# Kernel tuning notes

Measured on AMD Instinct MI355X. Metric: run time of the kernel, lower is better.

The kernel has to match this reference:

```python
import jax, jax.numpy as jnp
import numpy as np

LOG2PI = float(np.log(2.0 * np.pi))
T, S, D, K = 1024, 512, 32, 64


def setup_inputs() -> dict:
    key = jax.random.key(0)
    k0, k1, k2, k3, k4 = jax.random.split(key, 5)
    data = jax.random.normal(k0, (T, S, D), dtype=jnp.float32)  # packed time-major
    ip = jax.random.uniform(k1, (K,), dtype=jnp.float32)
    initial_probs = ip / ip.sum()
    A = jax.random.uniform(k2, (K, K), dtype=jnp.float32)
    transition_probs = A / A.sum(-1, keepdims=True)  # row-stochastic
    means = jax.random.normal(k3, (K, D), dtype=jnp.float32)
    covars = jax.random.uniform(k4, (K, D), dtype=jnp.float32) * 0.5 + 0.5  # positive diag
    return {"data": data, "initial_probs": initial_probs,
            "transition_probs": transition_probs, "means": means, "covars": covars}


def _emission_probs(data, means, covars):
    # Gaussian diag-covariance densities, [T, S, K], without materializing [T,S,K,D].
    inv = 1.0 / covars  # [K, D]
    quad = (jnp.einsum('tsd,kd->tsk', data * data, inv)
            - 2.0 * jnp.einsum('tsd,kd->tsk', data, means * inv)
            + (means * means * inv).sum(-1))  # [T, S, K]
    logp = -0.5 * (quad + jnp.log(covars).sum(-1) + data.shape[-1] * LOG2PI)
    return jnp.exp(logp)


def reference(data, initial_probs, transition_probs, means, covars):
    probs = _emission_probs(data, means, covars)  # [T, S, K]
    # t = 0: alpha = normalize(initial * emission)
    a0 = initial_probs * probs[0]
    d0 = a0.sum(-1, keepdims=True)
    alpha0 = a0 / d0
    log_denom0 = jnp.log(d0)  # [S, 1]

    def step(carry, p_t):
        alpha, log_denom = carry
        a = p_t * (alpha @ transition_probs)  # [S, K]
        d = a.sum(-1, keepdims=True)
        return (a / d, log_denom + jnp.log(d)), None

    (alpha, log_denom), _ = jax.lax.scan(step, (alpha0, log_denom0), probs[1:])
    log_likeli = jax.nn.logsumexp(jnp.log(alpha) + log_denom, axis=-1).sum()
    return alpha, -log_likeli
```

## Files before the change

kernel.cpp:

```cpp
#include <hip/hip_runtime.h>
#include <hip/hip_fp16.h>
#include <math.h>

#define TT 1024
#define SS 512
#define DD 32
#define KK 64

#define LOG2PI_F 1.8378770664093453f

#define QSEQ 16
#define NSEG 16
#define SEGLEN (TT / NSEG)
#define BURN 64

#define PBUF_BYTES ((size_t)TT * SS * KK * 2)
#define EM_WPB 4
#define EM_BLOCKS 2048
#define NWAVES (EM_BLOCKS * EM_WPB)

typedef float v2f __attribute__((ext_vector_type(2)));
typedef float f32x4 __attribute__((ext_vector_type(4)));
typedef _Float16 h8 __attribute__((ext_vector_type(8)));

__device__ __forceinline__ v2f fma2(v2f a, v2f b, v2f c) {
#if __has_builtin(__builtin_elementwise_fma)
    return __builtin_elementwise_fma(a, b, c);
#else
    v2f r; r.x = fmaf(a.x, b.x, c.x); r.y = fmaf(a.y, b.y, c.y); return r;
#endif
}

template <int CTRL, int RMASK>
__device__ __forceinline__ float dpp_max(float x) {
    int xi = __float_as_int(x);
    int t = __builtin_amdgcn_update_dpp(xi, xi, CTRL, RMASK, 0xf, false);
    return fmaxf(x, __int_as_float(t));
}
__device__ __forceinline__ float wave_reduce_max(float x) {
    x = dpp_max<0x111, 0xf>(x);
    x = dpp_max<0x112, 0xf>(x);
    x = dpp_max<0x114, 0xf>(x);
    x = dpp_max<0x118, 0xf>(x);
    x = dpp_max<0x142, 0xa>(x);
    x = dpp_max<0x143, 0xc>(x);
    return __int_as_float(__builtin_amdgcn_readlane(__float_as_int(x), 63));
}
template <int N>
__device__ __forceinline__ float dpp_ror_add(float x) {
    int xi = __float_as_int(x);
    int t = __builtin_amdgcn_update_dpp(xi, xi, 0x120 + N, 0xf, 0xf, false);
    return x + __int_as_float(t);
}
__device__ __forceinline__ float rowsum16(float x) {
    x = dpp_ror_add<8>(x);
    x = dpp_ror_add<4>(x);
    x = dpp_ror_add<2>(x);
    x = dpp_ror_add<1>(x);
    return x;
}

__global__ __launch_bounds__(EM_WPB * 64)
__attribute__((amdgpu_waves_per_eu(1, 3)))
void emission_kernel(
    const float* __restrict__ data,
    const float* __restrict__ means,
    const float* __restrict__ covars,
    __half* __restrict__ pbuf,
    float* __restrict__ mpart)
{
    const int k  = threadIdx.x & 63;
    const int w  = threadIdx.x >> 6;
    const int wv = blockIdx.x * EM_WPB + w;

    v2f w2[DD / 2], m2[DD / 2];
    float c0 = DD * LOG2PI_F;
#pragma unroll
    for (int d = 0; d < DD; ++d) {
        float c = covars[k * DD + d];
        ((float*)w2)[d] = 1.0f / c;
        ((float*)m2)[d] = means[k * DD + d];
        c0 += __logf(c);
    }

    __shared__ __align__(16) float4 xst[EM_WPB][2][64];

    const int base = wv * 64;
    const float4* dsrc = (const float4*)(data + (size_t)base * DD);

    float4 xr = dsrc[k];
    xst[w][0][k] = xr;
    __builtin_amdgcn_wave_barrier();

    float macc = 0.0f;
    int cur = 0;

    for (int b = 0; b < 8; ++b) {
        const int bn = (b + 1 < 8) ? (b + 1) : 7;
        xr = dsrc[bn * 64 + k];

        const float* xb = (const float*)&xst[w][cur][0];
#pragma unroll
        for (int i = 0; i < 8; i += 2) {
            const float4* x0q = (const float4*)(xb + i * DD);
            const float4* x1q = (const float4*)(xb + (i + 1) * DD);
            v2f p00 = {0,0}, p01 = {0,0}, p10 = {0,0}, p11 = {0,0};
#pragma unroll
            for (int d4 = 0; d4 < DD / 4; ++d4) {
                float4 x0 = x0q[d4];
                float4 x1 = x1q[d4];
                v2f xa0; xa0.x = x0.x; xa0.y = x0.y;
                v2f xb0; xb0.x = x0.z; xb0.y = x0.w;
                v2f xa1; xa1.x = x1.x; xa1.y = x1.y;
                v2f xb1; xb1.x = x1.z; xb1.y = x1.w;
                v2f ta0 = xa0 - m2[2 * d4],  tb0 = xb0 - m2[2 * d4 + 1];
                v2f ta1 = xa1 - m2[2 * d4],  tb1 = xb1 - m2[2 * d4 + 1];
                p00 = fma2(w2[2 * d4] * ta0, ta0, p00);
                p01 = fma2(w2[2 * d4 + 1] * tb0, tb0, p01);
                p10 = fma2(w2[2 * d4] * ta1, ta1, p10);
                p11 = fma2(w2[2 * d4 + 1] * tb1, tb1, p11);
            }
            v2f s0 = p00 + p01, s1 = p10 + p11;
            float logp0 = -0.5f * ((s0.x + s0.y) + c0);
            float logp1 = -0.5f * ((s1.x + s1.y) + c0);
            float mx0 = wave_reduce_max(logp0);
            float mx1 = wave_reduce_max(logp1);
            const int item0 = base + b * 8 + i;
            pbuf[(size_t)item0 * KK + k]       = __float2half(__expf(logp0 - mx0));
            pbuf[(size_t)(item0 + 1) * KK + k] = __float2half(__expf(logp1 - mx1));
            macc += mx0 + mx1;
        }

        xst[w][cur ^ 1][k] = xr;
        __builtin_amdgcn_wave_barrier();
        cur ^= 1;
    }
    if (k == 0) mpart[wv] = macc;
}

#define RSTR 72

__global__ __launch_bounds__(64)
__attribute__((amdgpu_waves_per_eu(1, 1)))
void hmm_mfma(
    const __half* __restrict__ pbuf,
    const float* __restrict__ initial,
    const float* __restrict__ trans,
    float* __restrict__ out_alpha,
    float* __restrict__ seq_logd)
{
    const int lane = threadIdx.x;
    const int col  = lane & 15;
    const int grp  = lane >> 4;
    const int s0   = blockIdx.x * QSEQ;
    const int seg  = blockIdx.y;

    const int emit_from = seg * SEGLEN;
    const int t0        = seg ? (emit_from - BURN) : 0;
    const int nsteps    = seg ? (SEGLEN + BURN) : SEGLEN;

    h8 bf[2][4];
#pragma unroll
    for (int kc = 0; kc < 2; ++kc)
#pragma unroll
        for (int nt = 0; nt < 4; ++nt) {
            h8 v;
#pragma unroll
            for (int e = 0; e < 8; ++e) {
                int j = kc * 32 + grp * 8 + e;
                v[e] = (_Float16)trans[j * KK + nt * 16 + col];
            }
            bf[kc][nt] = v;
        }

    float init_c[4];
#pragma unroll
    for (int nt = 0; nt < 4; ++nt)
        init_c[nt] = seg ? 1.0f : initial[nt * 16 + col];

    __shared__ __align__(16) _Float16 ash[QSEQ * RSTR];
    __shared__ __align__(16) _Float16 plds[2][4 * QSEQ * RSTR];

    float4 pr[8];
#define XLOAD(TB)                                                             \
    {                                                                         \
        const float4* src = (const float4*)(pbuf +                            \
            (((size_t)((TB) + grp)) * SS + s0 + col) * KK);                   \
        _Pragma("unroll")                                                     \
        for (int e = 0; e < 8; ++e) pr[e] = src[e];                           \
    }
#define XWRITE(BUF)                                                           \
    {                                                                         \
        float4* dst = (float4*)(&plds[BUF][(grp * 16 + col) * RSTR]);         \
        _Pragma("unroll")                                                     \
        for (int e = 0; e < 8; ++e) dst[e] = pr[e];                           \
    }

    XLOAD(t0);
    XWRITE(0);
    __builtin_amdgcn_wave_barrier();

    h8 a0, a1;
    float ld[4] = {0.0f, 0.0f, 0.0f, 0.0f};
    int cur = 0;

    for (int g = 0; g < nsteps / 4; ++g) {
        const int tbase = t0 + 4 * g;
        int tb_next = tbase + 4;
        if (tb_next > TT - 4) tb_next = TT - 4;
        XLOAD(tb_next);

        const _Float16* pc_base = &plds[cur][0];
#pragma unroll
        for (int st = 0; st < 4; ++st) {
            const int t = tbase + st;
            f32x4 c[4];
            if (g == 0 && st == 0) {
#pragma unroll
                for (int nt = 0; nt < 4; ++nt) {
                    f32x4 z = {init_c[nt], init_c[nt], init_c[nt], init_c[nt]};
                    c[nt] = z;
                }
            } else {
                f32x4 z = {0.0f, 0.0f, 0.0f, 0.0f};
#pragma unroll
                for (int nt = 0; nt < 4; ++nt) {
                    c[nt] = __builtin_amdgcn_mfma_f32_16x16x32_f16(
                        a0, bf[0][nt], z, 0, 0, 0);
                    c[nt] = __builtin_amdgcn_mfma_f32_16x16x32_f16(
                        a1, bf[1][nt], c[nt], 0, 0, 0);
                }
            }

            float av[4][4];
            float pden[4] = {0.0f, 0.0f, 0.0f, 0.0f};
#pragma unroll
            for (int nt = 0; nt < 4; ++nt)
#pragma unroll
                for (int j = 0; j < 4; ++j) {
                    float pcv = (float)pc_base[
                        (st * 16 + grp * 4 + j) * RSTR + nt * 16 + col];
                    float v = c[nt][j] * pcv;
                    av[nt][j] = v;
                    pden[j] += v;
                }

            float r[4];
#pragma unroll
            for (int j = 0; j < 4; ++j) {
                float den = rowsum16(pden[j]);
                if (t >= emit_from) ld[j] += __logf(den);
                r[j] = __builtin_amdgcn_rcpf(den);
            }

#pragma unroll
            for (int nt = 0; nt < 4; ++nt)
#pragma unroll
                for (int j = 0; j < 4; ++j)
                    ash[(grp * 4 + j) * RSTR + nt * 16 + col] =
                        (_Float16)(av[nt][j] * r[j]);
            __builtin_amdgcn_wave_barrier();
            a0 = *(const h8*)(ash + col * RSTR + grp * 8);
            a1 = *(const h8*)(ash + col * RSTR + 32 + grp * 8);
            __builtin_amdgcn_wave_barrier();
        }

        XWRITE(cur ^ 1);
        __builtin_amdgcn_wave_barrier();
        cur ^= 1;
    }
#undef XLOAD
#undef XWRITE

    if (seg == NSEG - 1) {
#pragma unroll
        for (int nt = 0; nt < 4; ++nt)
#pragma unroll
            for (int j = 0; j < 4; ++j)
                out_alpha[(size_t)(s0 + grp * 4 + j) * KK + nt * 16 + col] =
                    (float)ash[(grp * 4 + j) * RSTR + nt * 16 + col];
    }
    if (col == 0) {
#pragma unroll
        for (int j = 0; j < 4; ++j)
            seq_logd[seg * SS + s0 + grp * 4 + j] = ld[j];
    }
}

__global__ __launch_bounds__(256) void finalize(
    const float* __restrict__ seq_logd, const float* __restrict__ mpart,
    float* __restrict__ out_nll)
{
    float v = 0.0f;
    for (int j = threadIdx.x; j < NWAVES; j += 256) v += mpart[j];
    for (int j = threadIdx.x; j < NSEG * SS; j += 256) v += seq_logd[j];
#pragma unroll
    for (int off = 32; off > 0; off >>= 1)
        v += __shfl_xor(v, off, 64);
    __shared__ float sh[4];
    if ((threadIdx.x & 63) == 0) sh[threadIdx.x >> 6] = v;
    __syncthreads();
    if (threadIdx.x == 0) {
        double total = ((double)sh[0] + sh[1]) + ((double)sh[2] + sh[3]);
        out_nll[0] = (float)(-total);
    }
}

extern "C" void kernel_launch(void* const* d_in, const int* in_sizes, int n_in,
                              void* d_out, int out_size, void* d_ws, size_t ws_size,
                              hipStream_t stream) {
    const float* data    = (const float*)d_in[0];
    const float* initial = (const float*)d_in[1];
    const float* trans   = (const float*)d_in[2];
    const float* means   = (const float*)d_in[3];
    const float* covars  = (const float*)d_in[4];

    float* out_alpha = (float*)d_out;
    float* out_nll   = (float*)d_out + (size_t)SS * KK;

    __half* pbuf     = (__half*)d_ws;
    float*  mpart    = (float*)((char*)d_ws + PBUF_BYTES);
    float*  seq_logd = (float*)((char*)d_ws + PBUF_BYTES + NWAVES * sizeof(float));

    emission_kernel<<<EM_BLOCKS, EM_WPB * 64, 0, stream>>>(
        data, means, covars, pbuf, mpart);
    hmm_mfma<<<dim3(SS / QSEQ, NSEG), 64, 0, stream>>>(
        pbuf, initial, trans, out_alpha, seq_logd);
    finalize<<<1, 256, 0, stream>>>(seq_logd, mpart, out_nll);
}
```

Measured before the change: 287.6 us.

## Expand emission quadratic in log2 domain and double scan segments

The emission kernel now expands the Gaussian quadratic as x²·w + x·(m·w) + const, with the constants pre-scaled by log2(e). Squared inputs are staged in LDS alongside x, and exp2 is used, which removes the per-dimension subtraction and lets the log2-domain max offsets be converted back with ln2 at finalize. The scan splits time into 32 segments instead of 16 to give more parallel blocks. Each segment keeps its 64-step burn-in, so total recurrence work grows in exchange for shorter per-block critical paths. The expanded quadratic form may lose some precision through cancellation.

After: 275.1 us. 1.05x faster.

```diff
diff --git a/kernel.cpp b/kernel.cpp
--- a/kernel.cpp
+++ b/kernel.cpp
@@ -8,9 +8,11 @@
 #define KK 64
 
 #define LOG2PI_F 1.8378770664093453f
+#define L2E_F    1.4426950408889634f
+#define LN2_F    0.6931471805599453f
 
 #define QSEQ 16
-#define NSEG 16
+#define NSEG 32
 #define SEGLEN (TT / NSEG)
 #define BURN 64
 
@@ -28,6 +30,14 @@
     return __builtin_elementwise_fma(a, b, c);
 #else
     v2f r; r.x = fmaf(a.x, b.x, c.x); r.y = fmaf(a.y, b.y, c.y); return r;
+#endif
+}
+
+__device__ __forceinline__ float fast_exp2(float x) {
+#if __has_builtin(__builtin_amdgcn_exp2f)
+    return __builtin_amdgcn_exp2f(x);
+#else
+    return __expf(x * LN2_F);
 #endif
 }
 
@@ -73,23 +83,32 @@
     const int w  = threadIdx.x >> 6;
     const int wv = blockIdx.x * EM_WPB + w;
 
-    v2f w2[DD / 2], m2[DD / 2];
+    v2f W2[DD / 2], MW2[DD / 2];
     float c0 = DD * LOG2PI_F;
+    float mm = 0.0f;
 #pragma unroll
     for (int d = 0; d < DD; ++d) {
         float c = covars[k * DD + d];
-        ((float*)w2)[d] = 1.0f / c;
-        ((float*)m2)[d] = means[k * DD + d];
+        float m = means[k * DD + d];
+        float wi = 1.0f / c;
+        ((float*)W2)[d]  = -0.5f * L2E_F * wi;
+        ((float*)MW2)[d] = L2E_F * wi * m;
+        mm += m * m * wi;
         c0 += __logf(c);
     }
+    const float C = -0.5f * L2E_F * (c0 + mm);
 
     __shared__ __align__(16) float4 xst[EM_WPB][2][64];
+    __shared__ __align__(16) float4 sst[EM_WPB][2][64];
 
     const int base = wv * 64;
     const float4* dsrc = (const float4*)(data + (size_t)base * DD);
 
     float4 xr = dsrc[k];
+    float4 sr; sr.x = xr.x * xr.x; sr.y = xr.y * xr.y;
+    sr.z = xr.z * xr.z; sr.w = xr.w * xr.w;
     xst[w][0][k] = xr;
+    sst[w][0][k] = sr;
     __builtin_amdgcn_wave_barrier();
 
     float macc = 0.0f;
@@ -100,38 +119,38 @@
         xr = dsrc[bn * 64 + k];
 
         const float* xb = (const float*)&xst[w][cur][0];
-#pragma unroll
-        for (int i = 0; i < 8; i += 2) {
-            const float4* x0q = (const float4*)(xb + i * DD);
-            const float4* x1q = (const float4*)(xb + (i + 1) * DD);
-            v2f p00 = {0,0}, p01 = {0,0}, p10 = {0,0}, p11 = {0,0};
+        const float* sb = (const float*)&sst[w][cur][0];
+#pragma unroll
+        for (int i = 0; i < 8; ++i) {
+            const int item = base + b * 8 + i;
+            const float4* xq = (const float4*)(xb + i * DD);
+            const float4* sq = (const float4*)(sb + i * DD);
+            v2f qa = {C, 0.0f}, qb = {0.0f, 0.0f};
+            v2f qc = {0.0f, 0.0f}, qd = {0.0f, 0.0f};
 #pragma unroll
             for (int d4 = 0; d4 < DD / 4; ++d4) {
-                float4 x0 = x0q[d4];
-                float4 x1 = x1q[d4];
-                v2f xa0; xa0.x = x0.x; xa0.y = x0.y;
-                v2f xb0; xb0.x = x0.z; xb0.y = x0.w;
-                v2f xa1; xa1.x = x1.x; xa1.y = x1.y;
-                v2f xb1; xb1.x = x1.z; xb1.y = x1.w;
-                v2f ta0 = xa0 - m2[2 * d4],  tb0 = xb0 - m2[2 * d4 + 1];
-                v2f ta1 = xa1 - m2[2 * d4],  tb1 = xb1 - m2[2 * d4 + 1];
-                p00 = fma2(w2[2 * d4] * ta0, ta0, p00);
-                p01 = fma2(w2[2 * d4 + 1] * tb0, tb0, p01);
-                p10 = fma2(w2[2 * d4] * ta1, ta1, p10);
-                p11 = fma2(w2[2 * d4 + 1] * tb1, tb1, p11);
+                float4 xv = xq[d4];
+                float4 sv = sq[d4];
+                v2f x01; x01.x = xv.x; x01.y = xv.y;
+                v2f x23; x23.x = xv.z; x23.y = xv.w;
+                v2f s01; s01.x = sv.x; s01.y = sv.y;
+                v2f s23; s23.x = sv.z; s23.y = sv.w;
+                qa = fma2(s01, W2[2 * d4], qa);
+                qb = fma2(s23, W2[2 * d4 + 1], qb);
+                qc = fma2(x01, MW2[2 * d4], qc);
+                qd = fma2(x23, MW2[2 * d4 + 1], qd);
             }
-            v2f s0 = p00 + p01, s1 = p10 + p11;
-            float logp0 = -0.5f * ((s0.x + s0.y) + c0);
-            float logp1 = -0.5f * ((s1.x + s1.y) + c0);
-            float mx0 = wave_reduce_max(logp0);
-            float mx1 = wave_reduce_max(logp1);
-            const int item0 = base + b * 8 + i;
-            pbuf[(size_t)item0 * KK + k]       = __float2half(__expf(logp0 - mx0));
-            pbuf[(size_t)(item0 + 1) * KK + k] = __float2half(__expf(logp1 - mx1));
-            macc += mx0 + mx1;
+            v2f s = (qa + qb) + (qc + qd);
+            float logp2 = s.x + s.y;
+            float mx2 = wave_reduce_max(logp2);
+            pbuf[(size_t)item * KK + k] = __float2half(fast_exp2(logp2 - mx2));
+            macc += mx2;
         }
 
+        float4 s2; s2.x = xr.x * xr.x; s2.y = xr.y * xr.y;
+        s2.z = xr.z * xr.z; s2.w = xr.w * xr.w;
         xst[w][cur ^ 1][k] = xr;
+        sst[w][cur ^ 1][k] = s2;
         __builtin_amdgcn_wave_barrier();
         cur ^= 1;
     }
@@ -156,8 +175,8 @@
     const int seg  = blockIdx.y;
 
     const int emit_from = seg * SEGLEN;
-    const int t0        = seg ? (emit_from - BURN) : 0;
-    const int nsteps    = seg ? (SEGLEN + BURN) : SEGLEN;
+    int t0 = emit_from - BURN; if (t0 < 0) t0 = 0;
+    const int nsteps = (emit_from - t0) + SEGLEN;
 
     h8 bf[2][4];
 #pragma unroll
@@ -176,7 +195,7 @@
     float init_c[4];
 #pragma unroll
     for (int nt = 0; nt < 4; ++nt)
-        init_c[nt] = seg ? 1.0f : initial[nt * 16 + col];
+        init_c[nt] = (t0 == 0) ? initial[nt * 16 + col] : 1.0f;
 
     __shared__ __align__(16) _Float16 ash[QSEQ * RSTR];
     __shared__ __align__(16) _Float16 plds[2][4 * QSEQ * RSTR];
@@ -292,7 +311,7 @@
     float* __restrict__ out_nll)
 {
     float v = 0.0f;
-    for (int j = threadIdx.x; j < NWAVES; j += 256) v += mpart[j];
+    for (int j = threadIdx.x; j < NWAVES; j += 256) v += mpart[j] * LN2_F;
     for (int j = threadIdx.x; j < NSEG * SS; j += 256) v += seq_logd[j];
 #pragma unroll
     for (int off = 32; off > 0; off >>= 1)
```
